# Performance work log

Measured on AMD Instinct MI355X. Metric: run time of the kernel, lower is better.

The kernel has to match this reference:

```python
import jax, jax.numpy as jnp
import numpy as np

B, N0, C, H, T = 32, 513, 768, 12, 10
Dh = C // H
SCALE = Dh ** -0.5
HID = 4 * C  # mlp hidden


def _ln(x, g, b, eps=1e-5):
    m = jnp.mean(x, axis=-1, keepdims=True)
    v = jnp.mean((x - m) ** 2, axis=-1, keepdims=True)
    return (x - m) * jax.lax.rsqrt(v + eps) * g + b


def setup_inputs() -> dict:
    key = jax.random.key(0)
    ks = jax.random.split(key, 8)
    s = 0.02
    return {
        "x": jax.random.normal(ks[0], (B, N0, C), jnp.float32),
        "global_feature": jax.random.normal(ks[1], (B, 1, C), jnp.float32),
        "token_position": jax.random.normal(ks[2], (T, C), jnp.float32) * s,
        "prompt_emb": jax.random.normal(ks[3], (T, C), jnp.float32) * s,
        "scaler1": jnp.ones((1,), jnp.float32) * 0.3,
        "g1": jnp.ones((C,), jnp.float32),
        "b1": jnp.zeros((C,), jnp.float32),
        "w_qkv": jax.random.normal(ks[4], (3 * C, C), jnp.float32) * s,
        "w_proj": jax.random.normal(ks[5], (C, C), jnp.float32) * s,
        "b_proj": jnp.zeros((C,), jnp.float32),
        "g2": jnp.ones((C,), jnp.float32),
        "b2": jnp.zeros((C,), jnp.float32),
        "w_fc1": jax.random.normal(ks[6], (HID, C), jnp.float32) * s,
        "b_fc1": jnp.zeros((HID,), jnp.float32),
        "w_fc2": jax.random.normal(ks[7], (C, HID), jnp.float32) * s,
        "b_fc2": jnp.zeros((C,), jnp.float32),
    }


def reference(x, global_feature, token_position, prompt_emb, scaler1,
              g1, b1, w_qkv, w_proj, b_proj, g2, b2,
              w_fc1, b_fc1, w_fc2, b_fc2):
    # prompt-token fusion: [1,T,C] + [B,1,C] + [1,T,C] -> [B,T,C]
    token_prompt = prompt_emb[None] + scaler1 * global_feature + token_position[None]
    x = jnp.concatenate([x[:, :1], token_prompt, x[:, 1:]], axis=1)  # [B, N, C]
    Bx, N, _ = x.shape

    # attention branch
    h = _ln(x, g1, b1)
    qkv = h @ w_qkv.T  # [B, N, 3C]
    qkv = qkv.reshape(Bx, N, 3, H, Dh)
    q = qkv[:, :, 0].transpose(0, 2, 1, 3)  # [B, H, N, Dh]
    k = qkv[:, :, 1].transpose(0, 2, 1, 3)
    v = qkv[:, :, 2].transpose(0, 2, 1, 3)
    attn = jax.nn.softmax(jnp.einsum('bhqd,bhkd->bhqk', q, k) * SCALE, axis=-1)
    o = jnp.einsum('bhqk,bhkd->bhqd', attn, v).transpose(0, 2, 1, 3).reshape(Bx, N, C)
    x = x + o @ w_proj.T + b_proj

    # mlp branch (exact GELU as nn.GELU)
    h2 = _ln(x, g2, b2)
    x = x + jax.nn.gelu(h2 @ w_fc1.T + b_fc1, approximate=False) @ w_fc2.T + b_fc2
    return x
```

## Files before the change

### kernel.cpp

```cpp
#include <hip/hip_runtime.h>
#include <math.h>

typedef float  f32x4 __attribute__((ext_vector_type(4)));
typedef short  s16x8 __attribute__((ext_vector_type(8)));
typedef unsigned short u16;

#define DEVI static __device__ __forceinline__

constexpr int B_   = 32, N0_ = 513, C_ = 768, H_ = 12, T_ = 10;
constexpr int NSEQ = 523;
constexpr int M_   = B_ * NSEQ;
constexpr int HID_ = 3072;
constexpr float SCALE_ = 0.125f;
constexpr int NPAD = 576;

constexpr size_t OFF_A  = 25706496;
constexpr size_t OFF_VT = OFF_A + 77119488;
constexpr size_t OFF_O  = OFF_VT + 28311552;
constexpr size_t OFF_W  = OFF_O + 25706496;
constexpr size_t OFF_WQ = OFF_W;
constexpr size_t OFF_WP = OFF_WQ + 3538944;
constexpr size_t OFF_W1 = OFF_WP + 1179648;
constexpr size_t OFF_W2 = OFF_W1 + 4718592;

DEVI u16 f2bf(float f) {
  union { float f; unsigned u; } x; x.f = f;
  unsigned r = x.u + 0x7fffu + ((x.u >> 16) & 1u);
  return (u16)(r >> 16);
}

DEVI void async_ld16(const void* g, void* l) {
  __builtin_amdgcn_global_load_lds(
      (const __attribute__((address_space(1))) unsigned*)g,
      (__attribute__((address_space(3))) unsigned*)l, 16, 0, 0);
}

DEVI f32x4 mfma16(s16x8 a, s16x8 b, f32x4 c) {
  return __builtin_amdgcn_mfma_f32_16x16x32_bf16(a, b, c, 0, 0, 0);
}

__global__ void k_cvt(const float* __restrict__ in, u16* __restrict__ out, int n4) {
  int i = blockIdx.x * 256 + threadIdx.x;
  if (i >= n4) return;
  float4 v = reinterpret_cast<const float4*>(in)[i];
  ushort4 o;
  o.x = f2bf(v.x); o.y = f2bf(v.y); o.z = f2bf(v.z); o.w = f2bf(v.w);
  reinterpret_cast<ushort4*>(out)[i] = o;
}

__global__ void k_build(const float* __restrict__ x, const float* __restrict__ gf,
                        const float* __restrict__ tp, const float* __restrict__ pe,
                        const float* __restrict__ s1, float* __restrict__ xcat) {
  int i = blockIdx.x * 256 + threadIdx.x;
  if (i >= M_ * C_ / 4) return;
  int row = i / (C_ / 4), c4 = i % (C_ / 4);
  int b = row / NSEQ, n = row - b * NSEQ;
  float4 v;
  if (n == 0) {
    v = reinterpret_cast<const float4*>(x + (size_t)b * N0_ * C_)[c4];
  } else if (n <= T_) {
    int t = n - 1;
    float4 a  = reinterpret_cast<const float4*>(pe + (size_t)t * C_)[c4];
    float4 tv = reinterpret_cast<const float4*>(tp + (size_t)t * C_)[c4];
    float4 g  = reinterpret_cast<const float4*>(gf + (size_t)b * C_)[c4];
    float s = s1[0];
    v.x = a.x + s * g.x + tv.x; v.y = a.y + s * g.y + tv.y;
    v.z = a.z + s * g.z + tv.z; v.w = a.w + s * g.w + tv.w;
  } else {
    v = reinterpret_cast<const float4*>(x + ((size_t)b * N0_ + (n - T_)) * C_)[c4];
  }
  reinterpret_cast<float4*>(xcat + (size_t)row * C_)[c4] = v;
}

__global__ void k_ln(const float* __restrict__ xin, const float* __restrict__ g,
                     const float* __restrict__ bb, u16* __restrict__ hout) {
  int lane = threadIdx.x & 63, wid = threadIdx.x >> 6;
  int row = blockIdx.x * 4 + wid;
  const float4* xr = reinterpret_cast<const float4*>(xin + (size_t)row * C_);
  float4 v[3]; float s = 0.f, sq = 0.f;
#pragma unroll
  for (int c = 0; c < 3; ++c) {
    v[c] = xr[c * 64 + lane];
    s  += v[c].x + v[c].y + v[c].z + v[c].w;
    sq += v[c].x * v[c].x + v[c].y * v[c].y + v[c].z * v[c].z + v[c].w * v[c].w;
  }
#pragma unroll
  for (int m = 1; m < 64; m <<= 1) { s += __shfl_xor(s, m, 64); sq += __shfl_xor(sq, m, 64); }
  float mean = s * (1.f / C_);
  float rstd = rsqrtf(sq * (1.f / C_) - mean * mean + 1e-5f);
  ushort4* orow = reinterpret_cast<ushort4*>(hout + (size_t)row * C_);
#pragma unroll
  for (int c = 0; c < 3; ++c) {
    float4 gv = reinterpret_cast<const float4*>(g)[c * 64 + lane];
    float4 bv = reinterpret_cast<const float4*>(bb)[c * 64 + lane];
    ushort4 o;
    o.x = f2bf((v[c].x - mean) * rstd * gv.x + bv.x);
    o.y = f2bf((v[c].y - mean) * rstd * gv.y + bv.y);
    o.z = f2bf((v[c].z - mean) * rstd * gv.z + bv.z);
    o.w = f2bf((v[c].w - mean) * rstd * gv.w + bv.w);
    orow[c * 64 + lane] = o;
  }
}

template<int EPI, int NDIM, int KDIM, int BM, int BN>
__global__ __launch_bounds__(512, 2) void k_gemm(
    const u16* __restrict__ A, const u16* __restrict__ Bw,
    u16* __restrict__ outb, float* __restrict__ outf,
    const float* __restrict__ bias, const float* __restrict__ resid,
    u16* __restrict__ vT) {
  extern __shared__ __align__(16) char smem[];
  constexpr int NMB  = (M_ + BM - 1) / BM;
  constexpr int MI   = BM / 32;
  constexpr int NJ   = BN / 64;
  constexpr int BUFB = (BM + BN) * 128;
  constexpr int NT   = KDIM / 64;

  const int lane = threadIdx.x & 63, wid = threadIdx.x >> 6;
  const int wr = wid >> 2, wc = wid & 3;

  const int nwg = gridDim.x;
  const int q = nwg >> 3, r = nwg & 7;
  const int xcd = blockIdx.x & 7, sub = blockIdx.x >> 3;
  const int wgid = (xcd < r ? xcd * (q + 1) : r * (q + 1) + (xcd - r) * q) + sub;
  const int nb = wgid / NMB, mb = wgid - nb * NMB;
  const int m0 = mb * BM, n0 = nb * BN;

  auto stage = [&](int buf, int k0) {
    char* la = smem + buf * BUFB;
    char* lb = la + BM * 128;
#pragma unroll
    for (int jj = 0; jj < BM / 64; ++jj) {
      int j = jj * 8 + wid;
      int row = j * 8 + (lane >> 3);
      int gm = m0 + row; if (gm > M_ - 1) gm = M_ - 1;
      int cb = ((lane & 7) * 16) ^ ((row & 7) << 4);
      async_ld16((const char*)A + ((size_t)gm * KDIM + k0) * 2 + cb, la + j * 1024);
    }
#pragma unroll
    for (int jj = 0; jj < BN / 64; ++jj) {
      int j = jj * 8 + wid;
      int row = j * 8 + (lane >> 3);
      int cb = ((lane & 7) * 16) ^ ((row & 7) << 4);
      async_ld16((const char*)Bw + ((size_t)(n0 + row) * KDIM + k0) * 2 + cb,
                 lb + j * 1024);
    }
  };

  f32x4 acc[MI][NJ] = {};
  stage(0, 0);
  __syncthreads();
  int cur = 0;
#pragma unroll 1
  for (int t = 0; t < NT; ++t) {
    if (t + 1 < NT) stage(cur ^ 1, (t + 1) * 64);
    const char* la = smem + cur * BUFB;
    const char* lb = la + BM * 128;
#pragma unroll
    for (int kk = 0; kk < 2; ++kk) {
      s16x8 af[MI], bfr[NJ];
#pragma unroll
      for (int ii = 0; ii < MI; ++ii) {
        int row = wr * (BM / 2) + ii * 16 + (lane & 15);
        int cb = (kk * 64 + (lane >> 4) * 16) ^ ((row & 7) << 4);
        af[ii] = *reinterpret_cast<const s16x8*>(la + row * 128 + cb);
      }
#pragma unroll
      for (int jj = 0; jj < NJ; ++jj) {
        int row = wc * (BN / 4) + jj * 16 + (lane & 15);
        int cb = (kk * 64 + (lane >> 4) * 16) ^ ((row & 7) << 4);
        bfr[jj] = *reinterpret_cast<const s16x8*>(lb + row * 128 + cb);
      }
#pragma unroll
      for (int ii = 0; ii < MI; ++ii)
#pragma unroll
        for (int jj = 0; jj < NJ; ++jj)
          acc[ii][jj] = mfma16(af[ii], bfr[jj], acc[ii][jj]);
    }
    __syncthreads();
    cur ^= 1;
  }

#pragma unroll
  for (int ii = 0; ii < MI; ++ii) {
#pragma unroll
    for (int jj = 0; jj < NJ; ++jj) {
#pragma unroll
      for (int rr = 0; rr < 4; ++rr) {
        int gm = m0 + wr * (BM / 2) + ii * 16 + (lane >> 4) * 4 + rr;
        int gn = n0 + wc * (BN / 4) + jj * 16 + (lane & 15);
        if (gm < M_) {
          float v = acc[ii][jj][rr];
          if constexpr (EPI == 0) {
            u16 bv = f2bf(v);
            outb[(size_t)gm * NDIM + gn] = bv;
            if (gn >= 2 * C_) {
              int hh = (gn - 2 * C_) >> 6;
              int dh = gn & 63;
              int b2 = gm / NSEQ, nn = gm - b2 * NSEQ;
              vT[((size_t)(b2 * H_ + hh) * 64 + dh) * NPAD + nn] = bv;
            }
          } else if constexpr (EPI == 1) {
            size_t idx = (size_t)gm * NDIM + gn;
            outf[idx] = v + bias[gn] + resid[idx];
          } else {
            float t = v + bias[gn];
            outb[(size_t)gm * NDIM + gn] =
                f2bf(0.5f * t * (1.f + erff(t * 0.70710678118654752f)));
          }
        }
      }
    }
  }
}

__global__ __launch_bounds__(256) void k_attn(const u16* __restrict__ qkv,
                                              const u16* __restrict__ vT,
                                              u16* __restrict__ o) {
  __shared__ __align__(16) char lds[24576];
  const int qt = blockIdx.x, bh = blockIdx.y;
  const int b = bh / H_, h = bh - b * H_;
  const int lane = threadIdx.x & 63, wid = threadIdx.x >> 6;

  s16x8 qf[2];
  {
    int n = qt * 64 + wid * 16 + (lane & 15); if (n > NSEQ - 1) n = NSEQ - 1;
    const u16* qrow = qkv + (size_t)(b * NSEQ + n) * (3 * C_) + h * 64 + (lane >> 4) * 8;
    qf[0] = *reinterpret_cast<const s16x8*>(qrow);
    qf[1] = *reinterpret_cast<const s16x8*>(qrow + 32);
  }
  float m_run[4] = {-1e30f, -1e30f, -1e30f, -1e30f};
  float l_run[4] = {0.f, 0.f, 0.f, 0.f};
  f32x4 oacc[4] = {};
  char* pl = lds + 16384 + wid * 2048;

  for (int t = 0; t < 9; ++t) {
    const int kv0 = t * 64;
    __syncthreads();
#pragma unroll
    for (int jj = 0; jj < 2; ++jj) {
      int j = wid * 2 + jj;
      int row = j * 8 + (lane >> 3);
      int n = kv0 + row; if (n > NSEQ - 1) n = NSEQ - 1;
      int cb = ((lane & 7) * 16) ^ ((row & 7) << 4);
      async_ld16((const char*)(qkv + (size_t)(b * NSEQ + n) * (3 * C_) + C_ + h * 64) + cb,
                 lds + j * 1024);
    }
#pragma unroll
    for (int jj = 0; jj < 2; ++jj) {
      int j = wid * 2 + jj;
      int dh = j * 8 + (lane >> 3);
      int cb = ((lane & 7) * 16) ^ ((dh & 7) << 4);
      async_ld16((const char*)(vT + ((size_t)bh * 64 + dh) * NPAD + kv0) + cb,
                 lds + 8192 + j * 1024);
    }
    __syncthreads();

    f32x4 sfr[4] = {};
#pragma unroll
    for (int kk = 0; kk < 2; ++kk) {
#pragma unroll
      for (int fc = 0; fc < 4; ++fc) {
        int row = fc * 16 + (lane & 15);
        int cb = (kk * 64 + (lane >> 4) * 16) ^ ((row & 7) << 4);
        s16x8 kf = *reinterpret_cast<const s16x8*>(lds + row * 128 + cb);
        sfr[fc] = mfma16(qf[kk], kf, sfr[fc]);
      }
    }
#pragma unroll
    for (int fc = 0; fc < 4; ++fc) {
      bool valid = (kv0 + fc * 16 + (lane & 15)) < NSEQ;
#pragma unroll
      for (int rr = 0; rr < 4; ++rr)
        sfr[fc][rr] = valid ? sfr[fc][rr] * SCALE_ : -1e30f;
    }
#pragma unroll
    for (int rr = 0; rr < 4; ++rr) {
      float mx = fmaxf(fmaxf(sfr[0][rr], sfr[1][rr]), fmaxf(sfr[2][rr], sfr[3][rr]));
      mx = fmaxf(mx, __shfl_xor(mx, 1, 64));
      mx = fmaxf(mx, __shfl_xor(mx, 2, 64));
      mx = fmaxf(mx, __shfl_xor(mx, 4, 64));
      mx = fmaxf(mx, __shfl_xor(mx, 8, 64));
      float mnew = fmaxf(m_run[rr], mx);
      float sc = __expf(m_run[rr] - mnew);
      l_run[rr] *= sc;
#pragma unroll
      for (int f2 = 0; f2 < 4; ++f2) oacc[f2][rr] *= sc;
      float ps = 0.f;
#pragma unroll
      for (int fc = 0; fc < 4; ++fc) {
        float p = __expf(sfr[fc][rr] - mnew);
        sfr[fc][rr] = p; ps += p;
      }
      ps += __shfl_xor(ps, 1, 64);
      ps += __shfl_xor(ps, 2, 64);
      ps += __shfl_xor(ps, 4, 64);
      ps += __shfl_xor(ps, 8, 64);
      l_run[rr] += ps;
      m_run[rr] = mnew;
    }
#pragma unroll
    for (int fc = 0; fc < 4; ++fc)
#pragma unroll
      for (int rr = 0; rr < 4; ++rr) {
        int row = (lane >> 4) * 4 + rr;
        int cb = ((fc * 16 + (lane & 15)) * 2) ^ ((row & 7) << 4);
        *reinterpret_cast<u16*>(pl + row * 128 + cb) = f2bf(sfr[fc][rr]);
      }
    s16x8 pf[2];
#pragma unroll
    for (int ks = 0; ks < 2; ++ks) {
      int row = lane & 15;
      int cb = (ks * 64 + (lane >> 4) * 16) ^ ((row & 7) << 4);
      pf[ks] = *reinterpret_cast<const s16x8*>(pl + row * 128 + cb);
    }
#pragma unroll
    for (int f2 = 0; f2 < 4; ++f2)
#pragma unroll
      for (int ks = 0; ks < 2; ++ks) {
        int vrow = f2 * 16 + (lane & 15);
        int cb = (ks * 64 + (lane >> 4) * 16) ^ ((vrow & 7) << 4);
        s16x8 vf = *reinterpret_cast<const s16x8*>(lds + 8192 + vrow * 128 + cb);
        oacc[f2] = mfma16(pf[ks], vf, oacc[f2]);
      }
  }
#pragma unroll
  for (int f2 = 0; f2 < 4; ++f2)
#pragma unroll
    for (int rr = 0; rr < 4; ++rr) {
      int n = qt * 64 + wid * 16 + (lane >> 4) * 4 + rr;
      if (n < NSEQ) {
        float val = oacc[f2][rr] / l_run[rr];
        o[(size_t)(b * NSEQ + n) * C_ + h * 64 + f2 * 16 + (lane & 15)] = f2bf(val);
      }
    }
}

extern "C" void kernel_launch(void* const* d_in, const int* in_sizes, int n_in,
                              void* d_out, int out_size, void* d_ws, size_t ws_size,
                              hipStream_t stream) {
  const float* x    = (const float*)d_in[0];
  const float* gf   = (const float*)d_in[1];
  const float* tp   = (const float*)d_in[2];
  const float* pe   = (const float*)d_in[3];
  const float* s1   = (const float*)d_in[4];
  const float* g1   = (const float*)d_in[5];
  const float* b1   = (const float*)d_in[6];
  const float* wqkv = (const float*)d_in[7];
  const float* wproj= (const float*)d_in[8];
  const float* bproj= (const float*)d_in[9];
  const float* g2   = (const float*)d_in[10];
  const float* b2   = (const float*)d_in[11];
  const float* wfc1 = (const float*)d_in[12];
  const float* bfc1 = (const float*)d_in[13];
  const float* wfc2 = (const float*)d_in[14];
  const float* bfc2 = (const float*)d_in[15];

  char* ws = (char*)d_ws;
  u16* h    = (u16*)ws;
  u16* qkvb = (u16*)(ws + OFF_A);
  u16* hmid = qkvb;
  u16* vTb  = (u16*)(ws + OFF_VT);
  u16* ob   = (u16*)(ws + OFF_O);
  u16* wqb  = (u16*)(ws + OFF_WQ);
  u16* wpb  = (u16*)(ws + OFF_WP);
  u16* w1b  = (u16*)(ws + OFF_W1);
  u16* w2b  = (u16*)(ws + OFF_W2);
  float* xcat = (float*)d_out;

  constexpr int SH256 = (256 + 256) * 128 * 2;
  constexpr int SH128 = (256 + 128) * 128 * 2;
  (void)hipFuncSetAttribute((const void*)&k_gemm<0, 2304, 768, 256, 256>,
      hipFuncAttributeMaxDynamicSharedMemorySize, SH256);
  (void)hipFuncSetAttribute((const void*)&k_gemm<2, 3072, 768, 256, 256>,
      hipFuncAttributeMaxDynamicSharedMemorySize, SH256);
  (void)hipFuncSetAttribute((const void*)&k_gemm<1, 768, 768, 256, 128>,
      hipFuncAttributeMaxDynamicSharedMemorySize, SH128);
  (void)hipFuncSetAttribute((const void*)&k_gemm<1, 768, 3072, 256, 128>,
      hipFuncAttributeMaxDynamicSharedMemorySize, SH128);

  k_cvt<<<(442368 + 255) / 256, 256, 0, stream>>>(wqkv, wqb, 442368);
  k_cvt<<<(147456 + 255) / 256, 256, 0, stream>>>(wproj, wpb, 147456);
  k_cvt<<<(589824 + 255) / 256, 256, 0, stream>>>(wfc1, w1b, 589824);
  k_cvt<<<(589824 + 255) / 256, 256, 0, stream>>>(wfc2, w2b, 589824);

  k_build<<<(M_ * C_ / 4 + 255) / 256, 256, 0, stream>>>(x, gf, tp, pe, s1, xcat);
  k_ln<<<M_ / 4, 256, 0, stream>>>(xcat, g1, b1, h);
  k_gemm<0, 2304, 768, 256, 256><<<66 * 9, 512, SH256, stream>>>(
      h, wqb, qkvb, nullptr, nullptr, nullptr, vTb);
  k_attn<<<dim3(9, B_ * H_), 256, 0, stream>>>(qkvb, vTb, ob);
  k_gemm<1, 768, 768, 256, 128><<<66 * 6, 512, SH128, stream>>>(
      ob, wpb, nullptr, xcat, bproj, xcat, nullptr);
  k_ln<<<M_ / 4, 256, 0, stream>>>(xcat, g2, b2, h);
  k_gemm<2, 3072, 768, 256, 256><<<66 * 12, 512, SH256, stream>>>(
      h, w1b, hmid, nullptr, bfc1, nullptr, nullptr);
  k_gemm<1, 768, 3072, 256, 128><<<66 * 6, 512, SH128, stream>>>(
      hmid, w2b, nullptr, (float*)d_out, bfc2, xcat, nullptr);
}
```

Baseline: 850.8 us.

## Split GEMM K-tiles into half-stages with vmcnt-based waits and MFMA priority

Rewrites the GEMM main loop so each 64-wide K tile is staged and consumed as two 32-wide halves, with a new packed two-rows-per-128B LDS layout and XOR swizzle. The full __syncthreads is replaced by inline s_waitcnt vmcnt(N)+s_barrier, so the next half's async loads can stay in flight while the current half computes. MFMA sections are wrapped in s_setprio to favour matrix issue. The intent is finer-grained overlap of global-to-LDS loads with compute; the risk is that the hand-counted vmcnt values are wrong, which would give races or extra stalls.

New measurement: 853.0 us. About the same (+0.3%).

```diff
diff --git a/kernel.cpp b/kernel.cpp
--- a/kernel.cpp
+++ b/kernel.cpp
@@ -37,6 +37,16 @@
 
 DEVI f32x4 mfma16(s16x8 a, s16x8 b, f32x4 c) {
   return __builtin_amdgcn_mfma_f32_16x16x32_bf16(a, b, c, 0, 0, 0);
+}
+
+DEVI void wait_bar_v4() { asm volatile("s_waitcnt vmcnt(4)\n\ts_barrier" ::: "memory"); }
+DEVI void wait_bar_v3() { asm volatile("s_waitcnt vmcnt(3)\n\ts_barrier" ::: "memory"); }
+DEVI void wait_bar_v0() { asm volatile("s_waitcnt vmcnt(0)\n\ts_barrier" ::: "memory"); }
+template<int N> DEVI void wait_bar() {
+  static_assert(N == 4 || N == 3 || N == 0, "unsupported vmcnt");
+  if constexpr (N == 4) wait_bar_v4();
+  else if constexpr (N == 3) wait_bar_v3();
+  else wait_bar_v0();
 }
 
 __global__ void k_cvt(const float* __restrict__ in, u16* __restrict__ out, int n4) {
@@ -109,11 +119,14 @@
     const float* __restrict__ bias, const float* __restrict__ resid,
     u16* __restrict__ vT) {
   extern __shared__ __align__(16) char smem[];
-  constexpr int NMB  = (M_ + BM - 1) / BM;
-  constexpr int MI   = BM / 32;
-  constexpr int NJ   = BN / 64;
-  constexpr int BUFB = (BM + BN) * 128;
-  constexpr int NT   = KDIM / 64;
+  constexpr int NMB   = (M_ + BM - 1) / BM;
+  constexpr int MI    = BM / 32;
+  constexpr int NJ    = BN / 64;
+  constexpr int PA    = BM * 64;
+  constexpr int PB    = BN * 64;
+  constexpr int BUFB  = 2 * (PA + PB);
+  constexpr int NT    = KDIM / 64;
+  constexpr int WAITN = BM / 128 + BN / 128;
 
   const int lane = threadIdx.x & 63, wid = threadIdx.x >> 6;
   const int wr = wid >> 2, wc = wid & 3;
@@ -125,59 +138,76 @@
   const int nb = wgid / NMB, mb = wgid - nb * NMB;
   const int m0 = mb * BM, n0 = nb * BN;
 
-  auto stage = [&](int buf, int k0) {
-    char* la = smem + buf * BUFB;
-    char* lb = la + BM * 128;
-#pragma unroll
-    for (int jj = 0; jj < BM / 64; ++jj) {
-      int j = jj * 8 + wid;
-      int row = j * 8 + (lane >> 3);
+  auto stageAB = [&](int buf, int t, int kh) {
+    const int k0 = t * 64 + kh * 32;
+    char* base = smem + buf * BUFB;
+    char* pa = base + kh * PA;
+#pragma unroll
+    for (int sg = 0; sg < BM / 128; ++sg) {
+      int s = sg * 8 + wid;
+      int c = s * 64 + lane;
+      int lrow = c >> 3;
+      int jp = (c & 7) ^ (lrow & 7);
+      int row = lrow * 2 + (jp >> 2);
       int gm = m0 + row; if (gm > M_ - 1) gm = M_ - 1;
-      int cb = ((lane & 7) * 16) ^ ((row & 7) << 4);
-      async_ld16((const char*)A + ((size_t)gm * KDIM + k0) * 2 + cb, la + j * 1024);
-    }
-#pragma unroll
-    for (int jj = 0; jj < BN / 64; ++jj) {
-      int j = jj * 8 + wid;
-      int row = j * 8 + (lane >> 3);
-      int cb = ((lane & 7) * 16) ^ ((row & 7) << 4);
-      async_ld16((const char*)Bw + ((size_t)(n0 + row) * KDIM + k0) * 2 + cb,
-                 lb + j * 1024);
+      async_ld16((const char*)A + ((size_t)gm * KDIM + k0 + (jp & 3) * 8) * 2,
+                 pa + s * 1024);
+    }
+    char* pb = base + 2 * PA + kh * PB;
+#pragma unroll
+    for (int sg = 0; sg < BN / 128; ++sg) {
+      int s = sg * 8 + wid;
+      int c = s * 64 + lane;
+      int lrow = c >> 3;
+      int jp = (c & 7) ^ (lrow & 7);
+      int row = lrow * 2 + (jp >> 2);
+      async_ld16((const char*)Bw + ((size_t)(n0 + row) * KDIM + k0 + (jp & 3) * 8) * 2,
+                 pb + s * 1024);
     }
   };
 
   f32x4 acc[MI][NJ] = {};
-  stage(0, 0);
-  __syncthreads();
-  int cur = 0;
+
+  auto compute = [&](int buf, int kh) {
+    const char* base = smem + buf * BUFB;
+    const char* pa = base + kh * PA;
+    const char* pb = base + 2 * PA + kh * PB;
+    const int g = lane >> 4, r0 = lane & 15;
+    s16x8 af[MI], bfr[NJ];
+#pragma unroll
+    for (int ii = 0; ii < MI; ++ii) {
+      int rr = wr * (BM / 2) + ii * 16 + r0;
+      int lrow = rr >> 1;
+      int jp = (((rr & 1) << 2) | g) ^ (lrow & 7);
+      af[ii] = *reinterpret_cast<const s16x8*>(pa + lrow * 128 + jp * 16);
+    }
+#pragma unroll
+    for (int jn = 0; jn < NJ; ++jn) {
+      int rr = wc * (BN / 4) + jn * 16 + r0;
+      int lrow = rr >> 1;
+      int jp = (((rr & 1) << 2) | g) ^ (lrow & 7);
+      bfr[jn] = *reinterpret_cast<const s16x8*>(pb + lrow * 128 + jp * 16);
+    }
+    __builtin_amdgcn_s_setprio(1);
+#pragma unroll
+    for (int ii = 0; ii < MI; ++ii)
+#pragma unroll
+      for (int jn = 0; jn < NJ; ++jn)
+        acc[ii][jn] = mfma16(af[ii], bfr[jn], acc[ii][jn]);
+    __builtin_amdgcn_s_setprio(0);
+  };
+
+  stageAB(0, 0, 0);
+  stageAB(0, 0, 1);
 #pragma unroll 1
   for (int t = 0; t < NT; ++t) {
-    if (t + 1 < NT) stage(cur ^ 1, (t + 1) * 64);
-    const char* la = smem + cur * BUFB;
-    const char* lb = la + BM * 128;
-#pragma unroll
-    for (int kk = 0; kk < 2; ++kk) {
-      s16x8 af[MI], bfr[NJ];
-#pragma unroll
-      for (int ii = 0; ii < MI; ++ii) {
-        int row = wr * (BM / 2) + ii * 16 + (lane & 15);
-        int cb = (kk * 64 + (lane >> 4) * 16) ^ ((row & 7) << 4);
-        af[ii] = *reinterpret_cast<const s16x8*>(la + row * 128 + cb);
-      }
-#pragma unroll
-      for (int jj = 0; jj < NJ; ++jj) {
-        int row = wc * (BN / 4) + jj * 16 + (lane & 15);
-        int cb = (kk * 64 + (lane >> 4) * 16) ^ ((row & 7) << 4);
-        bfr[jj] = *reinterpret_cast<const s16x8*>(lb + row * 128 + cb);
-      }
-#pragma unroll
-      for (int ii = 0; ii < MI; ++ii)
-#pragma unroll
-        for (int jj = 0; jj < NJ; ++jj)
-          acc[ii][jj] = mfma16(af[ii], bfr[jj], acc[ii][jj]);
-    }
-    __syncthreads();
-    cur ^= 1;
+    const int p = t & 1;
+    wait_bar<WAITN>();
+    if (t + 1 < NT) stageAB(p ^ 1, t + 1, 0);
+    compute(p, 0);
+    if (t + 1 < NT) { wait_bar<WAITN>(); stageAB(p ^ 1, t + 1, 1); }
+    else            { wait_bar<0>(); }
+    compute(p, 1);
   }
 
 #pragma unroll
@@ -203,9 +233,9 @@
             size_t idx = (size_t)gm * NDIM + gn;
             outf[idx] = v + bias[gn] + resid[idx];
           } else {
-            float t = v + bias[gn];
+            float t2 = v + bias[gn];
             outb[(size_t)gm * NDIM + gn] =
-                f2bf(0.5f * t * (1.f + erff(t * 0.70710678118654752f)));
+                f2bf(0.5f * t2 * (1.f + erff(t2 * 0.70710678118654752f)));
           }
         }
       }
@@ -367,8 +397,8 @@
   u16* w2b  = (u16*)(ws + OFF_W2);
   float* xcat = (float*)d_out;
 
-  constexpr int SH256 = (256 + 256) * 128 * 2;
-  constexpr int SH128 = (256 + 128) * 128 * 2;
+  constexpr int SH256 = 2 * 2 * (256 * 64 + 256 * 64);
+  constexpr int SH128 = 2 * 2 * (256 * 64 + 128 * 64);
   (void)hipFuncSetAttribute((const void*)&k_gemm<0, 2304, 768, 256, 256>,
       hipFuncAttributeMaxDynamicSharedMemorySize, SH256);
   (void)hipFuncSetAttribute((const void*)&k_gemm<2, 3072, 768, 256, 256>,
```
